# Kernel tuning notes

Hardware: AMD Instinct MI355X
Metric: run time of the kernel (lower is better)

The kernel has to match this reference:

```python
import jax, jax.numpy as jnp
import numpy as np

DIM = 64  # matches init kwarg `dim`


def setup_inputs() -> dict:
    key = jax.random.key(0)
    k1, k2, k3, k4 = jax.random.split(key, 4)
    B, S, D = 16, 4096, DIM
    query = jax.random.normal(k1, (B, S, D), dtype=jnp.float32)
    key_t = jax.random.normal(k2, (B, S, D), dtype=jnp.float32)
    value = jax.random.normal(k3, (B, S, D), dtype=jnp.float32)
    mask = jax.random.randint(k4, (B, S), 0, 2).astype(jnp.bool_)
    return {"query": query, "key": key_t, "value": value, "mask": mask}


def reference(query, key, value, mask):
    # score: [B, Sq, Sk]
    scale = 1.0 / np.sqrt(DIM).astype(np.float32)
    score = jnp.einsum("bqd,bkd->bqk", query, key) * scale
    # mask reshaped to [B, 1, Sk]; True positions filled with -inf
    score = jnp.where(mask[:, None, :], -jnp.inf, score)
    attn = jax.nn.softmax(score, axis=-1)
    # dropout_p = 0.0 -> identity
    context = jnp.einsum("bqk,bkd->bqd", attn, value)
    return (context, attn)
```

## Files before the change

kernel.cpp:

```cpp
#include <hip/hip_runtime.h>
#include <hip/hip_bf16.h>
#include <cstdint>
#include <cstddef>

#define B_   16
#define S_   4096
#define D_   64
#define TQ   64
#define TK   64
#define NT   (S_ / TK)
#define KSTR 72
#define VSTR 72
#define PSTR 72
#define CTX_ELEMS (B_*S_*D_)

typedef __attribute__((ext_vector_type(8))) short short8;
typedef __attribute__((ext_vector_type(4))) float f32x4;

static __device__ __forceinline__ unsigned short f2bf(float f) {
  union { float f; unsigned int u; } v; v.f = f;
  unsigned int r = (v.u + 0x7FFFu + ((v.u >> 16) & 1u)) >> 16;
  return (unsigned short)r;
}

__global__ __launch_bounds__(256) void conv_bf16_kernel(
    const float* __restrict__ src, unsigned short* __restrict__ dst) {
  int i = blockIdx.x * 256 + threadIdx.x;
  const float4* s = (const float4*)src;
  float4 a = s[(size_t)i*2], b = s[(size_t)i*2 + 1];
  unsigned int u0 = (unsigned)f2bf(a.x) | ((unsigned)f2bf(a.y) << 16);
  unsigned int u1 = (unsigned)f2bf(a.z) | ((unsigned)f2bf(a.w) << 16);
  unsigned int u2 = (unsigned)f2bf(b.x) | ((unsigned)f2bf(b.y) << 16);
  unsigned int u3 = (unsigned)f2bf(b.z) | ((unsigned)f2bf(b.w) << 16);
  uint4 o; o.x = u0; o.y = u1; o.z = u2; o.w = u3;
  *(uint4*)(dst + (size_t)i * 8) = o;
}

__global__ __launch_bounds__(256) void convVt_kernel(
    const float* __restrict__ V, unsigned short* __restrict__ Vt) {
  __shared__ unsigned short lsT[D_ * VSTR];
  const int tid = threadIdx.x;
  const int b = blockIdx.y, k0 = blockIdx.x * 64;
  const float4* src = (const float4*)(V + ((size_t)(b * S_ + k0)) * D_);
#pragma unroll
  for (int i = 0; i < 4; ++i) {
    int li = tid + 256 * i;
    int row = li >> 4, c4 = li & 15;
    float4 v = src[row * 16 + c4];
    lsT[(c4 * 4 + 0) * VSTR + row] = f2bf(v.x);
    lsT[(c4 * 4 + 1) * VSTR + row] = f2bf(v.y);
    lsT[(c4 * 4 + 2) * VSTR + row] = f2bf(v.z);
    lsT[(c4 * 4 + 3) * VSTR + row] = f2bf(v.w);
  }
  __syncthreads();
#pragma unroll
  for (int i = 0; i < 2; ++i) {
    int li = tid + 256 * i;
    int d = li >> 3, c = li & 7;
    uint4 v = *(const uint4*)&lsT[d * VSTR + c * 8];
    *(uint4*)(Vt + ((size_t)(b * D_ + d)) * S_ + k0 + c * 8) = v;
  }
}

#define BAR_PLAIN() do { if constexpr (PRE) { \
    asm volatile("" ::: "memory"); \
    __builtin_amdgcn_s_barrier(); \
    asm volatile("" ::: "memory"); \
  } else { __syncthreads(); } } while (0)

#define BAR_LGKM() do { if constexpr (PRE) { \
    asm volatile("s_waitcnt lgkmcnt(0)" ::: "memory"); \
    __builtin_amdgcn_s_barrier(); \
    asm volatile("" ::: "memory"); \
  } else { __syncthreads(); } } while (0)

template<bool PRE>
__global__ __launch_bounds__(256, 3) void attn_kernel(
    const float* __restrict__ Q,
    const unsigned short* __restrict__ K16,
    const unsigned short* __restrict__ Vt16,
    const float* __restrict__ K32,
    const float* __restrict__ V32,
    const int* __restrict__ mask,
    float* __restrict__ out) {
  __shared__ unsigned short lsK[TK * KSTR];
  __shared__ unsigned short lsV[D_ * VSTR];
  __shared__ unsigned short lsP[4 * 16 * PSTR];
  __shared__ __align__(16) float lsBias[S_];

  const int tid = threadIdx.x;
  const int wave = tid >> 6, lane = tid & 63;
  const int quad = lane >> 4, n = lane & 15;

  const int g = blockIdx.x;
  const int b = (g & 7) * 2 + ((g >> 3) & 1);
  const int qt = g >> 4;
  const int qbase = qt * TQ;
  const int bS = b * S_;

  {
    const uint4* mi = (const uint4*)(mask + bS);
    float4* bo = (float4*)lsBias;
    for (int i = tid; i < S_ / 4; i += 256) {
      uint4 m = mi[i];
      float4 f;
      f.x = m.x ? -1e30f : 0.0f;
      f.y = m.y ? -1e30f : 0.0f;
      f.z = m.z ? -1e30f : 0.0f;
      f.w = m.w ? -1e30f : 0.0f;
      bo[i] = f;
    }
  }

  const float QSC = 0.125f * 1.44269504088896340736f;
  const int qrow = qbase + wave * 16 + n;
  const float* qp = Q + ((size_t)(bS + qrow)) * D_ + quad * 8;
  short8 aq0, aq1;
  {
    float4 f0 = *(const float4*)(qp);
    float4 f1 = *(const float4*)(qp + 4);
    float4 f2 = *(const float4*)(qp + 32);
    float4 f3 = *(const float4*)(qp + 36);
    aq0[0] = (short)f2bf(f0.x * QSC); aq0[1] = (short)f2bf(f0.y * QSC);
    aq0[2] = (short)f2bf(f0.z * QSC); aq0[3] = (short)f2bf(f0.w * QSC);
    aq0[4] = (short)f2bf(f1.x * QSC); aq0[5] = (short)f2bf(f1.y * QSC);
    aq0[6] = (short)f2bf(f1.z * QSC); aq0[7] = (short)f2bf(f1.w * QSC);
    aq1[0] = (short)f2bf(f2.x * QSC); aq1[1] = (short)f2bf(f2.y * QSC);
    aq1[2] = (short)f2bf(f2.z * QSC); aq1[3] = (short)f2bf(f2.w * QSC);
    aq1[4] = (short)f2bf(f3.x * QSC); aq1[5] = (short)f2bf(f3.y * QSC);
    aq1[6] = (short)f2bf(f3.z * QSC); aq1[7] = (short)f2bf(f3.w * QSC);
  }

  const int r0 = tid >> 3, c0 = tid & 7;

  uint4 sk0, sk1, sv0, sv1;

  float l0 = 0.f, l1 = 0.f, l2 = 0.f, l3 = 0.f;
  if constexpr (PRE) {
    sk0 = *(const uint4*)(K16 + ((size_t)(bS + r0)) * D_ + c0 * 8);
    sk1 = *(const uint4*)(K16 + ((size_t)(bS + r0 + 32)) * D_ + c0 * 8);
  }
  for (int kt = 0; kt < NT; ++kt) {
    const int k0 = kt * TK;
    BAR_PLAIN();
    if constexpr (PRE) {
      *(uint4*)&lsK[r0 * KSTR + c0 * 8] = sk0;
      *(uint4*)&lsK[(r0 + 32) * KSTR + c0 * 8] = sk1;
      if (kt + 1 < NT) {
        sk0 = *(const uint4*)(K16 + ((size_t)(bS + k0 + TK + r0)) * D_ + c0 * 8);
        sk1 = *(const uint4*)(K16 + ((size_t)(bS + k0 + TK + r0 + 32)) * D_ + c0 * 8);
      }
    } else {
#pragma unroll
      for (int i = 0; i < 4; ++i) {
        int li = tid + 256 * i;
        int row = li >> 4, c4 = li & 15;
        float4 v = *(const float4*)(K32 + ((size_t)(bS + k0 + row)) * D_ + c4 * 4);
        unsigned int u0 = (unsigned)f2bf(v.x) | ((unsigned)f2bf(v.y) << 16);
        unsigned int u1 = (unsigned)f2bf(v.z) | ((unsigned)f2bf(v.w) << 16);
        uint2 uu; uu.x = u0; uu.y = u1;
        *(uint2*)&lsK[row * KSTR + c4 * 4] = uu;
      }
    }
    BAR_LGKM();
#pragma unroll
    for (int ch = 0; ch < 4; ++ch) {
      short8 kb0 = *(const short8*)&lsK[(ch * 16 + n) * KSTR + quad * 8];
      short8 kb1 = *(const short8*)&lsK[(ch * 16 + n) * KSTR + 32 + quad * 8];
      f32x4 c = {0.f, 0.f, 0.f, 0.f};
      c = __builtin_amdgcn_mfma_f32_16x16x32_bf16(kb0, aq0, c, 0, 0, 0);
      c = __builtin_amdgcn_mfma_f32_16x16x32_bf16(kb1, aq1, c, 0, 0, 0);
      const float4 bb = *(const float4*)&lsBias[k0 + ch * 16 + quad * 4];
      l0 += exp2f(c[0] + bb.x);
      l1 += exp2f(c[1] + bb.y);
      l2 += exp2f(c[2] + bb.z);
      l3 += exp2f(c[3] + bb.w);
    }
  }
  if constexpr (PRE) {
    sk0 = *(const uint4*)(K16 + ((size_t)(bS + r0)) * D_ + c0 * 8);
    sk1 = *(const uint4*)(K16 + ((size_t)(bS + r0 + 32)) * D_ + c0 * 8);
    sv0 = *(const uint4*)(Vt16 + ((size_t)(b * D_ + r0)) * S_ + c0 * 8);
    sv1 = *(const uint4*)(Vt16 + ((size_t)(b * D_ + r0 + 32)) * S_ + c0 * 8);
  }
  float lt = (l0 + l1) + (l2 + l3);
  lt += __shfl_xor(lt, 16);
  lt += __shfl_xor(lt, 32);
  const float rl = 1.0f / lt;

  f32x4 oc0 = {0.f,0.f,0.f,0.f}, oc1 = {0.f,0.f,0.f,0.f};
  f32x4 oc2 = {0.f,0.f,0.f,0.f}, oc3 = {0.f,0.f,0.f,0.f};
  float* attnRow = out + CTX_ELEMS + ((size_t)(bS + qrow)) * S_;
  for (int kt = 0; kt < NT; ++kt) {
    const int k0 = kt * TK;
    BAR_PLAIN();
    if constexpr (PRE) {
      *(uint4*)&lsK[r0 * KSTR + c0 * 8] = sk0;
      *(uint4*)&lsK[(r0 + 32) * KSTR + c0 * 8] = sk1;
      *(uint4*)&lsV[r0 * VSTR + c0 * 8] = sv0;
      *(uint4*)&lsV[(r0 + 32) * VSTR + c0 * 8] = sv1;
      if (kt + 1 < NT) {
        sk0 = *(const uint4*)(K16 + ((size_t)(bS + k0 + TK + r0)) * D_ + c0 * 8);
        sk1 = *(const uint4*)(K16 + ((size_t)(bS + k0 + TK + r0 + 32)) * D_ + c0 * 8);
        sv0 = *(const uint4*)(Vt16 + ((size_t)(b * D_ + r0)) * S_ + k0 + TK + c0 * 8);
        sv1 = *(const uint4*)(Vt16 + ((size_t)(b * D_ + r0 + 32)) * S_ + k0 + TK + c0 * 8);
      }
    } else {
#pragma unroll
      for (int i = 0; i < 4; ++i) {
        int li = tid + 256 * i;
        int row = li >> 4, c4 = li & 15;
        float4 v = *(const float4*)(K32 + ((size_t)(bS + k0 + row)) * D_ + c4 * 4);
        unsigned int u0 = (unsigned)f2bf(v.x) | ((unsigned)f2bf(v.y) << 16);
        unsigned int u1 = (unsigned)f2bf(v.z) | ((unsigned)f2bf(v.w) << 16);
        uint2 uu; uu.x = u0; uu.y = u1;
        *(uint2*)&lsK[row * KSTR + c4 * 4] = uu;
        float4 vv = *(const float4*)(V32 + ((size_t)(bS + k0 + row)) * D_ + c4 * 4);
        lsV[(c4 * 4 + 0) * VSTR + row] = f2bf(vv.x);
        lsV[(c4 * 4 + 1) * VSTR + row] = f2bf(vv.y);
        lsV[(c4 * 4 + 2) * VSTR + row] = f2bf(vv.z);
        lsV[(c4 * 4 + 3) * VSTR + row] = f2bf(vv.w);
      }
    }
    BAR_LGKM();
#pragma unroll
    for (int ch = 0; ch < 4; ++ch) {
      short8 kb0 = *(const short8*)&lsK[(ch * 16 + n) * KSTR + quad * 8];
      short8 kb1 = *(const short8*)&lsK[(ch * 16 + n) * KSTR + 32 + quad * 8];
      f32x4 c = {0.f, 0.f, 0.f, 0.f};
      c = __builtin_amdgcn_mfma_f32_16x16x32_bf16(kb0, aq0, c, 0, 0, 0);
      c = __builtin_amdgcn_mfma_f32_16x16x32_bf16(kb1, aq1, c, 0, 0, 0);
      const float4 bb = *(const float4*)&lsBias[k0 + ch * 16 + quad * 4];
      f32x4 p;
      p[0] = exp2f(c[0] + bb.x) * rl;
      p[1] = exp2f(c[1] + bb.y) * rl;
      p[2] = exp2f(c[2] + bb.z) * rl;
      p[3] = exp2f(c[3] + bb.w) * rl;
      __builtin_nontemporal_store(p, (f32x4*)(attnRow + k0 + ch * 16 + quad * 4));
      uint2 pw;
      pw.x = (unsigned)f2bf(p[0]) | ((unsigned)f2bf(p[1]) << 16);
      pw.y = (unsigned)f2bf(p[2]) | ((unsigned)f2bf(p[3]) << 16);
      *(uint2*)&lsP[(wave * 16 + n) * PSTR + ch * 16 + quad * 4] = pw;
    }
#pragma unroll
    for (int ks = 0; ks < 2; ++ks) {
      short8 ap = *(const short8*)&lsP[(wave * 16 + n) * PSTR + ks * 32 + quad * 8];
      short8 bv0 = *(const short8*)&lsV[(0 * 16 + n) * VSTR + ks * 32 + quad * 8];
      short8 bv1 = *(const short8*)&lsV[(1 * 16 + n) * VSTR + ks * 32 + quad * 8];
      short8 bv2 = *(const short8*)&lsV[(2 * 16 + n) * VSTR + ks * 32 + quad * 8];
      short8 bv3 = *(const short8*)&lsV[(3 * 16 + n) * VSTR + ks * 32 + quad * 8];
      oc0 = __builtin_amdgcn_mfma_f32_16x16x32_bf16(ap, bv0, oc0, 0, 0, 0);
      oc1 = __builtin_amdgcn_mfma_f32_16x16x32_bf16(ap, bv1, oc1, 0, 0, 0);
      oc2 = __builtin_amdgcn_mfma_f32_16x16x32_bf16(ap, bv2, oc2, 0, 0, 0);
      oc3 = __builtin_amdgcn_mfma_f32_16x16x32_bf16(ap, bv3, oc3, 0, 0, 0);
    }
  }
#pragma unroll
  for (int r = 0; r < 4; ++r) {
    int qr = qbase + wave * 16 + quad * 4 + r;
    float* op = out + ((size_t)(bS + qr)) * D_ + n;
    __builtin_nontemporal_store(oc0[r], op + 0);
    __builtin_nontemporal_store(oc1[r], op + 16);
    __builtin_nontemporal_store(oc2[r], op + 32);
    __builtin_nontemporal_store(oc3[r], op + 48);
  }
}

extern "C" void kernel_launch(void* const* d_in, const int* in_sizes, int n_in,
                              void* d_out, int out_size, void* d_ws, size_t ws_size,
                              hipStream_t stream) {
  const float* q = (const float*)d_in[0];
  const float* k = (const float*)d_in[1];
  const float* v = (const float*)d_in[2];
  const int* mask = (const int*)d_in[3];
  float* out = (float*)d_out;

  const size_t elems = (size_t)B_ * S_ * D_;
  const size_t need = 2 * elems * sizeof(unsigned short);
  if (ws_size >= need) {
    unsigned short* K16 = (unsigned short*)d_ws;
    unsigned short* Vt16 = K16 + elems;
    conv_bf16_kernel<<<(int)(elems / 8 / 256), 256, 0, stream>>>(k, K16);
    convVt_kernel<<<dim3(S_ / 64, B_), 256, 0, stream>>>(v, Vt16);
    attn_kernel<true><<<B_ * (S_ / TQ), 256, 0, stream>>>(
        q, K16, Vt16, k, v, mask, out);
  } else {
    attn_kernel<false><<<B_ * (S_ / TQ), 256, 0, stream>>>(
        q, nullptr, nullptr, k, v, mask, out);
  }
}
```

Measured before the change: 1.289 ms.

## Load bf16 K and V fragments directly from global memory, dropping LDS staging

The precomputed-bf16 path no longer stages K and transposed V tiles through shared memory with block barriers. Each wave now loads its MFMA operand fragments straight from global memory (relying on L2/L1 caching), and uses only a per-wave LDS buffer for P with an lgkmcnt wait. LDS use drops to the bias and P buffers, so launch bounds rise to 4 blocks per SM. The intent is to remove barrier and LDS-copy overhead and raise occupancy, at the cost of redundant global/L2 traffic, since every wave refetches the same K/V rows.

```diff
diff --git a/kernel.cpp b/kernel.cpp
--- a/kernel.cpp
+++ b/kernel.cpp
@@ -62,29 +62,12 @@
   }
 }
 
-#define BAR_PLAIN() do { if constexpr (PRE) { \
-    asm volatile("" ::: "memory"); \
-    __builtin_amdgcn_s_barrier(); \
-    asm volatile("" ::: "memory"); \
-  } else { __syncthreads(); } } while (0)
-
-#define BAR_LGKM() do { if constexpr (PRE) { \
-    asm volatile("s_waitcnt lgkmcnt(0)" ::: "memory"); \
-    __builtin_amdgcn_s_barrier(); \
-    asm volatile("" ::: "memory"); \
-  } else { __syncthreads(); } } while (0)
-
-template<bool PRE>
-__global__ __launch_bounds__(256, 3) void attn_kernel(
+__global__ __launch_bounds__(256, 4) void attn_pre_kernel(
     const float* __restrict__ Q,
     const unsigned short* __restrict__ K16,
     const unsigned short* __restrict__ Vt16,
-    const float* __restrict__ K32,
-    const float* __restrict__ V32,
     const int* __restrict__ mask,
     float* __restrict__ out) {
-  __shared__ unsigned short lsK[TK * KSTR];
-  __shared__ unsigned short lsV[D_ * VSTR];
   __shared__ unsigned short lsP[4 * 16 * PSTR];
   __shared__ __align__(16) float lsBias[S_];
 
@@ -131,38 +114,155 @@
     aq1[6] = (short)f2bf(f3.z * QSC); aq1[7] = (short)f2bf(f3.w * QSC);
   }
 
-  const int r0 = tid >> 3, c0 = tid & 7;
-
-  uint4 sk0, sk1, sv0, sv1;
+  __syncthreads();
+
+  const unsigned short* kb = K16 + ((size_t)bS + n) * D_ + quad * 8;
 
   float l0 = 0.f, l1 = 0.f, l2 = 0.f, l3 = 0.f;
-  if constexpr (PRE) {
-    sk0 = *(const uint4*)(K16 + ((size_t)(bS + r0)) * D_ + c0 * 8);
-    sk1 = *(const uint4*)(K16 + ((size_t)(bS + r0 + 32)) * D_ + c0 * 8);
-  }
+  for (int kt = 0; kt < NT; ++kt) {
+    const unsigned short* kp = kb + (size_t)(kt * TK) * D_;
+    const float4* bp = (const float4*)&lsBias[kt * TK + quad * 4];
+#pragma unroll
+    for (int ch = 0; ch < 4; ++ch) {
+      short8 kb0 = *(const short8*)(kp + ch * 16 * D_);
+      short8 kb1 = *(const short8*)(kp + ch * 16 * D_ + 32);
+      f32x4 c = {0.f, 0.f, 0.f, 0.f};
+      c = __builtin_amdgcn_mfma_f32_16x16x32_bf16(kb0, aq0, c, 0, 0, 0);
+      c = __builtin_amdgcn_mfma_f32_16x16x32_bf16(kb1, aq1, c, 0, 0, 0);
+      const float4 bb = bp[ch * 4];
+      l0 += exp2f(c[0] + bb.x);
+      l1 += exp2f(c[1] + bb.y);
+      l2 += exp2f(c[2] + bb.z);
+      l3 += exp2f(c[3] + bb.w);
+    }
+  }
+  float lt = (l0 + l1) + (l2 + l3);
+  lt += __shfl_xor(lt, 16);
+  lt += __shfl_xor(lt, 32);
+  const float rl = 1.0f / lt;
+
+  f32x4 oc0 = {0.f,0.f,0.f,0.f}, oc1 = {0.f,0.f,0.f,0.f};
+  f32x4 oc2 = {0.f,0.f,0.f,0.f}, oc3 = {0.f,0.f,0.f,0.f};
+  float* attnRow = out + CTX_ELEMS + ((size_t)(bS + qrow)) * S_;
+  const unsigned short* vb = Vt16 + ((size_t)(b * D_) + n) * S_ + quad * 8;
+  const int prow = (wave * 16 + n) * PSTR;
+  for (int kt = 0; kt < NT; ++kt) {
+    asm volatile("" ::: "memory");
+    const int k0 = kt * TK;
+    const unsigned short* kp = kb + (size_t)k0 * D_;
+#pragma unroll
+    for (int ch = 0; ch < 4; ++ch) {
+      short8 kb0 = *(const short8*)(kp + ch * 16 * D_);
+      short8 kb1 = *(const short8*)(kp + ch * 16 * D_ + 32);
+      f32x4 c = {0.f, 0.f, 0.f, 0.f};
+      c = __builtin_amdgcn_mfma_f32_16x16x32_bf16(kb0, aq0, c, 0, 0, 0);
+      c = __builtin_amdgcn_mfma_f32_16x16x32_bf16(kb1, aq1, c, 0, 0, 0);
+      const float4 bb = *(const float4*)&lsBias[k0 + ch * 16 + quad * 4];
+      f32x4 p;
+      p[0] = exp2f(c[0] + bb.x) * rl;
+      p[1] = exp2f(c[1] + bb.y) * rl;
+      p[2] = exp2f(c[2] + bb.z) * rl;
+      p[3] = exp2f(c[3] + bb.w) * rl;
+      __builtin_nontemporal_store(p, (f32x4*)(attnRow + k0 + ch * 16 + quad * 4));
+      uint2 pw;
+      pw.x = (unsigned)f2bf(p[0]) | ((unsigned)f2bf(p[1]) << 16);
+      pw.y = (unsigned)f2bf(p[2]) | ((unsigned)f2bf(p[3]) << 16);
+      *(uint2*)&lsP[prow + ch * 16 + quad * 4] = pw;
+    }
+    asm volatile("s_waitcnt lgkmcnt(0)" ::: "memory");
+#pragma unroll
+    for (int ks = 0; ks < 2; ++ks) {
+      short8 ap = *(const short8*)&lsP[prow + ks * 32 + quad * 8];
+      short8 bv0 = *(const short8*)(vb + (size_t)(0 * 16) * S_ + k0 + ks * 32);
+      short8 bv1 = *(const short8*)(vb + (size_t)(1 * 16) * S_ + k0 + ks * 32);
+      short8 bv2 = *(const short8*)(vb + (size_t)(2 * 16) * S_ + k0 + ks * 32);
+      short8 bv3 = *(const short8*)(vb + (size_t)(3 * 16) * S_ + k0 + ks * 32);
+      oc0 = __builtin_amdgcn_mfma_f32_16x16x32_bf16(ap, bv0, oc0, 0, 0, 0);
+      oc1 = __builtin_amdgcn_mfma_f32_16x16x32_bf16(ap, bv1, oc1, 0, 0, 0);
+      oc2 = __builtin_amdgcn_mfma_f32_16x16x32_bf16(ap, bv2, oc2, 0, 0, 0);
+      oc3 = __builtin_amdgcn_mfma_f32_16x16x32_bf16(ap, bv3, oc3, 0, 0, 0);
+    }
+  }
+#pragma unroll
+  for (int r = 0; r < 4; ++r) {
+    int qr = qbase + wave * 16 + quad * 4 + r;
+    float* op = out + ((size_t)(bS + qr)) * D_ + n;
+    __builtin_nontemporal_store(oc0[r], op + 0);
+    __builtin_nontemporal_store(oc1[r], op + 16);
+    __builtin_nontemporal_store(oc2[r], op + 32);
+    __builtin_nontemporal_store(oc3[r], op + 48);
+  }
+}
+
+__global__ __launch_bounds__(256, 2) void attn_fb_kernel(
+    const float* __restrict__ Q,
+    const float* __restrict__ K32,
+    const float* __restrict__ V32,
+    const int* __restrict__ mask,
+    float* __restrict__ out) {
+  __shared__ unsigned short lsK[TK * KSTR];
+  __shared__ unsigned short lsV[D_ * VSTR];
+  __shared__ unsigned short lsP[4 * 16 * PSTR];
+  __shared__ __align__(16) float lsBias[S_];
+
+  const int tid = threadIdx.x;
+  const int wave = tid >> 6, lane = tid & 63;
+  const int quad = lane >> 4, n = lane & 15;
+
+  const int g = blockIdx.x;
+  const int b = (g & 7) * 2 + ((g >> 3) & 1);
+  const int qt = g >> 4;
+  const int qbase = qt * TQ;
+  const int bS = b * S_;
+
+  {
+    const uint4* mi = (const uint4*)(mask + bS);
+    float4* bo = (float4*)lsBias;
+    for (int i = tid; i < S_ / 4; i += 256) {
+      uint4 m = mi[i];
+      float4 f;
+      f.x = m.x ? -1e30f : 0.0f;
+      f.y = m.y ? -1e30f : 0.0f;
+      f.z = m.z ? -1e30f : 0.0f;
+      f.w = m.w ? -1e30f : 0.0f;
+      bo[i] = f;
+    }
+  }
+
+  const float QSC = 0.125f * 1.44269504088896340736f;
+  const int qrow = qbase + wave * 16 + n;
+  const float* qp = Q + ((size_t)(bS + qrow)) * D_ + quad * 8;
+  short8 aq0, aq1;
+  {
+    float4 f0 = *(const float4*)(qp);
+    float4 f1 = *(const float4*)(qp + 4);
+    float4 f2 = *(const float4*)(qp + 32);
+    float4 f3 = *(const float4*)(qp + 36);
+    aq0[0] = (short)f2bf(f0.x * QSC); aq0[1] = (short)f2bf(f0.y * QSC);
+    aq0[2] = (short)f2bf(f0.z * QSC); aq0[3] = (short)f2bf(f0.w * QSC);
+    aq0[4] = (short)f2bf(f1.x * QSC); aq0[5] = (short)f2bf(f1.y * QSC);
+    aq0[6] = (short)f2bf(f1.z * QSC); aq0[7] = (short)f2bf(f1.w * QSC);
+    aq1[0] = (short)f2bf(f2.x * QSC); aq1[1] = (short)f2bf(f2.y * QSC);
+    aq1[2] = (short)f2bf(f2.z * QSC); aq1[3] = (short)f2bf(f2.w * QSC);
+    aq1[4] = (short)f2bf(f3.x * QSC); aq1[5] = (short)f2bf(f3.y * QSC);
+    aq1[6] = (short)f2bf(f3.z * QSC); aq1[7] = (short)f2bf(f3.w * QSC);
+  }
+
+  float l0 = 0.f, l1 = 0.f, l2 = 0.f, l3 = 0.f;
   for (int kt = 0; kt < NT; ++kt) {
     const int k0 = kt * TK;
-    BAR_PLAIN();
-    if constexpr (PRE) {
-      *(uint4*)&lsK[r0 * KSTR + c0 * 8] = sk0;
-      *(uint4*)&lsK[(r0 + 32) * KSTR + c0 * 8] = sk1;
-      if (kt + 1 < NT) {
-        sk0 = *(const uint4*)(K16 + ((size_t)(bS + k0 + TK + r0)) * D_ + c0 * 8);
-        sk1 = *(const uint4*)(K16 + ((size_t)(bS + k0 + TK + r0 + 32)) * D_ + c0 * 8);
-      }
-    } else {
-#pragma unroll
-      for (int i = 0; i < 4; ++i) {
-        int li = tid + 256 * i;
-        int row = li >> 4, c4 = li & 15;
-        float4 v = *(const float4*)(K32 + ((size_t)(bS + k0 + row)) * D_ + c4 * 4);
-        unsigned int u0 = (unsigned)f2bf(v.x) | ((unsigned)f2bf(v.y) << 16);
-        unsigned int u1 = (unsigned)f2bf(v.z) | ((unsigned)f2bf(v.w) << 16);
-        uint2 uu; uu.x = u0; uu.y = u1;
-        *(uint2*)&lsK[row * KSTR + c4 * 4] = uu;
-      }
-    }
-    BAR_LGKM();
+    __syncthreads();
+#pragma unroll
+    for (int i = 0; i < 4; ++i) {
+      int li = tid + 256 * i;
+      int row = li >> 4, c4 = li & 15;
+      float4 v = *(const float4*)(K32 + ((size_t)(bS + k0 + row)) * D_ + c4 * 4);
+      unsigned int u0 = (unsigned)f2bf(v.x) | ((unsigned)f2bf(v.y) << 16);
+      unsigned int u1 = (unsigned)f2bf(v.z) | ((unsigned)f2bf(v.w) << 16);
+      uint2 uu; uu.x = u0; uu.y = u1;
+      *(uint2*)&lsK[row * KSTR + c4 * 4] = uu;
+    }
+    __syncthreads();
 #pragma unroll
     for (int ch = 0; ch < 4; ++ch) {
       short8 kb0 = *(const short8*)&lsK[(ch * 16 + n) * KSTR + quad * 8];
@@ -177,12 +277,6 @@
       l3 += exp2f(c[3] + bb.w);
     }
   }
-  if constexpr (PRE) {
-    sk0 = *(const uint4*)(K16 + ((size_t)(bS + r0)) * D_ + c0 * 8);
-    sk1 = *(const uint4*)(K16 + ((size_t)(bS + r0 + 32)) * D_ + c0 * 8);
-    sv0 = *(const uint4*)(Vt16 + ((size_t)(b * D_ + r0)) * S_ + c0 * 8);
-    sv1 = *(const uint4*)(Vt16 + ((size_t)(b * D_ + r0 + 32)) * S_ + c0 * 8);
-  }
   float lt = (l0 + l1) + (l2 + l3);
   lt += __shfl_xor(lt, 16);
   lt += __shfl_xor(lt, 32);
@@ -193,36 +287,23 @@
   float* attnRow = out + CTX_ELEMS + ((size_t)(bS + qrow)) * S_;
   for (int kt = 0; kt < NT; ++kt) {
     const int k0 = kt * TK;
-    BAR_PLAIN();
-    if constexpr (PRE) {
-      *(uint4*)&lsK[r0 * KSTR + c0 * 8] = sk0;
-      *(uint4*)&lsK[(r0 + 32) * KSTR + c0 * 8] = sk1;
-      *(uint4*)&lsV[r0 * VSTR + c0 * 8] = sv0;
-      *(uint4*)&lsV[(r0 + 32) * VSTR + c0 * 8] = sv1;
-      if (kt + 1 < NT) {
-        sk0 = *(const uint4*)(K16 + ((size_t)(bS + k0 + TK + r0)) * D_ + c0 * 8);
-        sk1 = *(const uint4*)(K16 + ((size_t)(bS + k0 + TK + r0 + 32)) * D_ + c0 * 8);
-        sv0 = *(const uint4*)(Vt16 + ((size_t)(b * D_ + r0)) * S_ + k0 + TK + c0 * 8);
-        sv1 = *(const uint4*)(Vt16 + ((size_t)(b * D_ + r0 + 32)) * S_ + k0 + TK + c0 * 8);
-      }
-    } else {
-#pragma unroll
-      for (int i = 0; i < 4; ++i) {
-        int li = tid + 256 * i;
-        int row = li >> 4, c4 = li & 15;
-        float4 v = *(const float4*)(K32 + ((size_t)(bS + k0 + row)) * D_ + c4 * 4);
-        unsigned int u0 = (unsigned)f2bf(v.x) | ((unsigned)f2bf(v.y) << 16);
-        unsigned int u1 = (unsigned)f2bf(v.z) | ((unsigned)f2bf(v.w) << 16);
-        uint2 uu; uu.x = u0; uu.y = u1;
-        *(uint2*)&lsK[row * KSTR + c4 * 4] = uu;
-        float4 vv = *(const float4*)(V32 + ((size_t)(bS + k0 + row)) * D_ + c4 * 4);
-        lsV[(c4 * 4 + 0) * VSTR + row] = f2bf(vv.x);
-        lsV[(c4 * 4 + 1) * VSTR + row] = f2bf(vv.y);
-        lsV[(c4 * 4 + 2) * VSTR + row] = f2bf(vv.z);
-        lsV[(c4 * 4 + 3) * VSTR + row] = f2bf(vv.w);
-      }
-    }
-    BAR_LGKM();
+    __syncthreads();
+#pragma unroll
+    for (int i = 0; i < 4; ++i) {
+      int li = tid + 256 * i;
+      int row = li >> 4, c4 = li & 15;
+      float4 v = *(const float4*)(K32 + ((size_t)(bS + k0 + row)) * D_ + c4 * 4);
+      unsigned int u0 = (unsigned)f2bf(v.x) | ((unsigned)f2bf(v.y) << 16);
+      unsigned int u1 = (unsigned)f2bf(v.z) | ((unsigned)f2bf(v.w) << 16);
+      uint2 uu; uu.x = u0; uu.y = u1;
+      *(uint2*)&lsK[row * KSTR + c4 * 4] = uu;
+      float4 vv = *(const float4*)(V32 + ((size_t)(bS + k0 + row)) * D_ + c4 * 4);
+      lsV[(c4 * 4 + 0) * VSTR + row] = f2bf(vv.x);
+      lsV[(c4 * 4 + 1) * VSTR + row] = f2bf(vv.y);
+      lsV[(c4 * 4 + 2) * VSTR + row] = f2bf(vv.z);
+      lsV[(c4 * 4 + 3) * VSTR + row] = f2bf(vv.w);
+    }
+    __syncthreads();
 #pragma unroll
     for (int ch = 0; ch < 4; ++ch) {
       short8 kb0 = *(const short8*)&lsK[(ch * 16 + n) * KSTR + quad * 8];
@@ -242,6 +323,7 @@
       pw.y = (unsigned)f2bf(p[2]) | ((unsigned)f2bf(p[3]) << 16);
       *(uint2*)&lsP[(wave * 16 + n) * PSTR + ch * 16 + quad * 4] = pw;
     }
+    asm volatile("s_waitcnt lgkmcnt(0)" ::: "memory");
 #pragma unroll
     for (int ks = 0; ks < 2; ++ks) {
       short8 ap = *(const short8*)&lsP[(wave * 16 + n) * PSTR + ks * 32 + quad * 8];
@@ -282,10 +364,10 @@
     unsigned short* Vt16 = K16 + elems;
     conv_bf16_kernel<<<(int)(elems / 8 / 256), 256, 0, stream>>>(k, K16);
     convVt_kernel<<<dim3(S_ / 64, B_), 256, 0, stream>>>(v, Vt16);
-    attn_kernel<true><<<B_ * (S_ / TQ), 256, 0, stream>>>(
-        q, K16, Vt16, k, v, mask, out);
+    attn_pre_kernel<<<B_ * (S_ / TQ), 256, 0, stream>>>(
+        q, K16, Vt16, mask, out);
   } else {
-    attn_kernel<false><<<B_ * (S_ / TQ), 256, 0, stream>>>(
-        q, nullptr, nullptr, k, v, mask, out);
-  }
-}
+    attn_fb_kernel<<<B_ * (S_ / TQ), 256, 0, stream>>>(
+        q, k, v, mask, out);
+  }
+}
```

Result: slower. 1.613 ms (+25.1%).
